# Kernel tuning notes

Hardware: AMD Instinct MI355X
Metric: run time of the kernel (lower is better)

The kernel has to match this reference:

```python
import jax, jax.numpy as jnp
import numpy as np

N_NODES = 100000
N_EDGES = 640000
H = 128

def setup_inputs() -> dict:
    key = jax.random.key(0)
    k = jax.random.split(key, 8)
    x_src = jax.random.normal(k[0], (N_NODES, H), dtype=jnp.float32)
    x_dst = jax.random.normal(k[1], (N_NODES, H), dtype=jnp.float32)
    src_idx = jax.random.randint(k[2], (N_EDGES,), 0, N_NODES, dtype=jnp.int64)
    dst_idx = jax.random.randint(k[3], (N_EDGES,), 0, N_NODES, dtype=jnp.int64)
    # torch Linear default init: U(-1/sqrt(fan_in), 1/sqrt(fan_in)); randn*scale is fine for a numeric baseline
    W1 = jax.random.normal(k[4], (H, 2 * H), dtype=jnp.float32) * (1.0 / np.sqrt(2 * H))
    b1 = jnp.zeros((H,), dtype=jnp.float32)
    W2 = jax.random.normal(k[5], (1, H), dtype=jnp.float32) * (1.0 / np.sqrt(H))
    b2 = jnp.zeros((1,), dtype=jnp.float32)
    return {"x_src": x_src, "x_dst": x_dst, "src_idx": src_idx, "dst_idx": dst_idx,
            "W1": W1, "b1": b1, "W2": W2, "b2": b2}

def reference(x_src, x_dst, src_idx, dst_idx, W1, b1, W2, b2):
    # per-edge gather of endpoint features, concat -> [E, 2H]
    h = jnp.concatenate([x_src[src_idx], x_dst[dst_idx]], axis=1)
    h = jax.nn.relu(h @ W1.T + b1)            # [E, H]
    score = (h @ W2.T + b2)[:, 0]             # [E]
    return score
```

## Files before the change

kernel.cpp:

```cpp
#include <hip/hip_runtime.h>
#include <hip/hip_bf16.h>

typedef __bf16 bf16x8 __attribute__((ext_vector_type(8)));
typedef __bf16 bf16x4 __attribute__((ext_vector_type(4)));
typedef float  f32x4  __attribute__((ext_vector_type(4)));

#define HF 128
#define W1K 256

__global__ __launch_bounds__(256, 2) void node_precompute3(
    const float* __restrict__ x_src, const float* __restrict__ x_dst,
    const float* __restrict__ W1,
    __bf16* __restrict__ u, __bf16* __restrict__ v, int nNodes)
{
    const int tid  = threadIdx.x;
    const int lane = tid & 63;
    const int wid  = tid >> 6;
    const int l15  = lane & 15;
    const int lg   = lane >> 4;

    const int gw     = blockIdx.x * 4 + wid;
    const int half   = gw & 1;
    const int stride = gridDim.x * 2;

    const float* __restrict__ x = half ? x_dst : x_src;
    const float* __restrict__ Wh = W1 + (half ? HF : 0);
    __bf16* __restrict__ outp = half ? v : u;

    bf16x8 wfrag[32];
    #pragma unroll
    for (int f = 0; f < 32; ++f) {
        const int mt = f >> 2;
        const int kk = f & 3;
        const float* p = Wh + (size_t)(mt * 16 + l15) * W1K + kk * 32 + lg * 8;
        f32x4 a = *reinterpret_cast<const f32x4*>(p);
        f32x4 b = *reinterpret_cast<const f32x4*>(p + 4);
        bf16x8 w8;
        #pragma unroll
        for (int i = 0; i < 4; ++i) {
            w8[i]     = (__bf16)a[i];
            w8[i + 4] = (__bf16)b[i];
        }
        wfrag[f] = w8;
    }

    const int nst = (nNodes + 15) >> 4;
    const size_t laneoff = (size_t)l15 * HF + lg * 8;

    int st = gw >> 1;
    if (st >= nst) return;

    f32x4 nxt[8];
    {
        const int node = min(st * 16 + l15, nNodes - 1);
        const float* rp = x + (size_t)node * HF + lg * 8;
        #pragma unroll
        for (int kk = 0; kk < 4; ++kk) {
            nxt[2 * kk]     = *reinterpret_cast<const f32x4*>(rp + kk * 32);
            nxt[2 * kk + 1] = *reinterpret_cast<const f32x4*>(rp + kk * 32 + 4);
        }
    }

    while (st < nst) {
        const int st2 = st + stride;

        bf16x8 xb[4];
        #pragma unroll
        for (int kk = 0; kk < 4; ++kk) {
            bf16x8 t;
            #pragma unroll
            for (int i = 0; i < 4; ++i) {
                t[i]     = (__bf16)nxt[2 * kk][i];
                t[i + 4] = (__bf16)nxt[2 * kk + 1][i];
            }
            xb[kk] = t;
        }

        if (st2 < nst) {
            const int node = min(st2 * 16 + l15, nNodes - 1);
            const float* rp = x + (size_t)node * HF + lg * 8;
            #pragma unroll
            for (int kk = 0; kk < 4; ++kk) {
                nxt[2 * kk]     = *reinterpret_cast<const f32x4*>(rp + kk * 32);
                nxt[2 * kk + 1] = *reinterpret_cast<const f32x4*>(rp + kk * 32 + 4);
            }
        }

        f32x4 acc[8];
        #pragma unroll
        for (int mt = 0; mt < 8; ++mt) acc[mt] = (f32x4){0.f, 0.f, 0.f, 0.f};

        #pragma unroll
        for (int kk = 0; kk < 4; ++kk)
            #pragma unroll
            for (int mt = 0; mt < 8; ++mt)
                acc[mt] = __builtin_amdgcn_mfma_f32_16x16x32_bf16(
                    wfrag[mt * 4 + kk], xb[kk], acc[mt], 0, 0, 0);

        const int mynode = st * 16 + l15;
        if (mynode < nNodes) {
            __bf16* op = outp + (size_t)mynode * HF + lg * 4;
            #pragma unroll
            for (int mt = 0; mt < 8; ++mt) {
                bf16x4 o4;
                #pragma unroll
                for (int r = 0; r < 4; ++r) o4[r] = (__bf16)acc[mt][r];
                *reinterpret_cast<bf16x4*>(op + mt * 16) = o4;
            }
        }
        st = st2;
    }
}

__global__ __launch_bounds__(256) void edge_score_kernel(
    const __bf16* __restrict__ u, const __bf16* __restrict__ v,
    const int* __restrict__ sidx, const int* __restrict__ didx,
    const float* __restrict__ W2, const float* __restrict__ b1,
    const float* __restrict__ b2,
    float* __restrict__ out, int nEdges)
{
    const int tid = threadIdx.x;
    const int sub = tid >> 4;
    const int l16 = tid & 15;

    const int ebase = blockIdx.x * 64 + sub;

    float w2v[8], b1v[8];
    #pragma unroll
    for (int j = 0; j < 8; ++j) {
        w2v[j] = W2[l16 * 8 + j];
        b1v[j] = b1[l16 * 8 + j];
    }
    const float b2v = b2[0];

    int e[4], si[4], di[4];
    #pragma unroll
    for (int q = 0; q < 4; ++q) {
        e[q] = ebase + q * 16;
        const int c = min(e[q], nEdges - 1);
        si[q] = sidx[c];
        di[q] = didx[c];
    }

    bf16x8 uv[4], vv[4];
    #pragma unroll
    for (int q = 0; q < 4; ++q) {
        uv[q] = *reinterpret_cast<const bf16x8*>(u + (size_t)si[q] * HF + l16 * 8);
        vv[q] = *reinterpret_cast<const bf16x8*>(v + (size_t)di[q] * HF + l16 * 8);
    }

    float s[4] = {0.f, 0.f, 0.f, 0.f};
    #pragma unroll
    for (int q = 0; q < 4; ++q)
        #pragma unroll
        for (int j = 0; j < 8; ++j)
            s[q] += fmaxf((float)uv[q][j] + (float)vv[q][j] + b1v[j], 0.f) * w2v[j];

    #pragma unroll
    for (int off = 1; off < 16; off <<= 1)
        #pragma unroll
        for (int q = 0; q < 4; ++q)
            s[q] += __shfl_xor(s[q], off, 64);

    if (l16 == 0) {
        #pragma unroll
        for (int q = 0; q < 4; ++q)
            if (e[q] < nEdges) out[e[q]] = s[q] + b2v;
    }
}

__global__ __launch_bounds__(256, 2) void edge_mlp_kernel(
    const float* __restrict__ x_src, const float* __restrict__ x_dst,
    const int*   __restrict__ src_idx, const int* __restrict__ dst_idx,
    const float* __restrict__ W1, const float* __restrict__ b1,
    const float* __restrict__ W2, const float* __restrict__ b2,
    float* __restrict__ out, int nEdges)
{
    __shared__ __align__(16) __bf16 w1lds[64 * 64 * 8];

    const int tid  = threadIdx.x;
    const int lane = tid & 63;
    const int wid  = tid >> 6;
    const int l15  = lane & 15;
    const int lg   = lane >> 4;

    for (int p = wid; p < 64; p += 4) {
        const int n   = p >> 3;
        const int kk  = p & 7;
        const float* src = W1 + (n * 16 + l15) * W1K + kk * 32 + lg * 8;
        bf16x8 w8;
        #pragma unroll
        for (int i = 0; i < 8; ++i) w8[i] = (__bf16)src[i];
        *reinterpret_cast<bf16x8*>(&w1lds[(p * 64 + lane) * 8]) = w8;
    }
    __syncthreads();

    float w2v[8], b1v[8];
    #pragma unroll
    for (int n = 0; n < 8; ++n) {
        w2v[n] = W2[n * 16 + l15];
        b1v[n] = b1[n * 16 + l15];
    }
    const float b2v = b2[0];

    const int ntiles = nEdges / 256;
    for (int t = blockIdx.x; t < ntiles; t += gridDim.x) {
        const int ebase = t * 256 + wid * 64;

        const float* srow[4];
        const float* drow[4];
        #pragma unroll
        for (int m = 0; m < 4; ++m) {
            const int e  = ebase + m * 16 + l15;
            srow[m] = x_src + (size_t)src_idx[e] * HF + lg * 8;
            drow[m] = x_dst + (size_t)dst_idx[e] * HF + lg * 8;
        }

        f32x4 acc[4][8];
        #pragma unroll
        for (int m = 0; m < 4; ++m)
            #pragma unroll
            for (int n = 0; n < 8; ++n)
                acc[m][n] = (f32x4){0.f, 0.f, 0.f, 0.f};

        #pragma unroll
        for (int kk = 0; kk < 8; ++kk) {
            bf16x8 a[4];
            #pragma unroll
            for (int m = 0; m < 4; ++m) {
                const float* p = (kk < 4) ? (srow[m] + kk * 32)
                                          : (drow[m] + (kk - 4) * 32);
                f32x4 u0 = *reinterpret_cast<const f32x4*>(p);
                f32x4 u1 = *reinterpret_cast<const f32x4*>(p + 4);
                bf16x8 av;
                #pragma unroll
                for (int i = 0; i < 4; ++i) {
                    av[i]     = (__bf16)u0[i];
                    av[i + 4] = (__bf16)u1[i];
                }
                a[m] = av;
            }
            #pragma unroll
            for (int n = 0; n < 8; ++n) {
                bf16x8 bfrag = *reinterpret_cast<const bf16x8*>(
                    &w1lds[((n * 8 + kk) * 64 + lane) * 8]);
                #pragma unroll
                for (int m = 0; m < 4; ++m) {
                    acc[m][n] = __builtin_amdgcn_mfma_f32_16x16x32_bf16(
                        a[m], bfrag, acc[m][n], 0, 0, 0);
                }
            }
        }

        #pragma unroll
        for (int m = 0; m < 4; ++m) {
            float part[4];
            #pragma unroll
            for (int r = 0; r < 4; ++r) {
                float s = 0.f;
                #pragma unroll
                for (int n = 0; n < 8; ++n) {
                    float hv = acc[m][n][r] + b1v[n];
                    s += fmaxf(hv, 0.f) * w2v[n];
                }
                part[r] = s;
            }
            #pragma unroll
            for (int off = 1; off < 16; off <<= 1) {
                #pragma unroll
                for (int r = 0; r < 4; ++r)
                    part[r] += __shfl_xor(part[r], off, 64);
            }
            if (l15 == m) {
                f32x4 v4 = { part[0] + b2v, part[1] + b2v,
                             part[2] + b2v, part[3] + b2v };
                *reinterpret_cast<f32x4*>(&out[ebase + m * 16 + lg * 4]) = v4;
            }
        }
    }
}

extern "C" void kernel_launch(void* const* d_in, const int* in_sizes, int n_in,
                              void* d_out, int out_size, void* d_ws, size_t ws_size,
                              hipStream_t stream) {
    const float* x_src  = (const float*)d_in[0];
    const float* x_dst  = (const float*)d_in[1];
    const int*   sidx   = (const int*)d_in[2];
    const int*   didx   = (const int*)d_in[3];
    const float* W1     = (const float*)d_in[4];
    const float* b1     = (const float*)d_in[5];
    const float* W2     = (const float*)d_in[6];
    const float* b2     = (const float*)d_in[7];
    float* out = (float*)d_out;

    const int nEdges = in_sizes[2];
    const int nNodes = in_sizes[0] / HF;

    const size_t needed = (size_t)2 * nNodes * HF * sizeof(__bf16);
    if (ws_size >= needed) {
        __bf16* u = (__bf16*)d_ws;
        __bf16* v = u + (size_t)nNodes * HF;

        node_precompute3<<<512, 256, 0, stream>>>(
            x_src, x_dst, W1, u, v, nNodes);

        const int egrid = (nEdges + 63) / 64;
        edge_score_kernel<<<egrid, 256, 0, stream>>>(
            u, v, sidx, didx, W2, b1, b2, out, nEdges);
    } else {
        edge_mlp_kernel<<<512, 256, 0, stream>>>(
            x_src, x_dst, sidx, didx, W1, b1, W2, b2, out, nEdges);
    }
}
```

Before: 86.35 us.

## Stage bf16 W1 fragments in LDS and use 512-thread node precompute blocks

Moves the bf16 weight fragments for both halves of W1 out of per-wave registers into shared memory, loaded once per block. The block grows to 8 waves, and each wave takes interleaved src/dst node tiles. Dropping 32 register fragments per lane is meant to raise occupancy and hide the latency of the streaming node-feature loads. In exchange, every MFMA now needs an LDS read of its A operand, and the fast path is limited to node counts divisible by 16, which drops the tail clamping.

```diff
diff --git a/kernel.cpp b/kernel.cpp
--- a/kernel.cpp
+++ b/kernel.cpp
@@ -8,31 +8,25 @@
 #define HF 128
 #define W1K 256
 
-__global__ __launch_bounds__(256, 2) void node_precompute3(
+__global__ __launch_bounds__(512, 4) void node_precompute4(
     const float* __restrict__ x_src, const float* __restrict__ x_dst,
     const float* __restrict__ W1,
     __bf16* __restrict__ u, __bf16* __restrict__ v, int nNodes)
 {
+    __shared__ __align__(16) __bf16 wlds[64 * 64 * 8];
+
     const int tid  = threadIdx.x;
     const int lane = tid & 63;
     const int wid  = tid >> 6;
     const int l15  = lane & 15;
     const int lg   = lane >> 4;
 
-    const int gw     = blockIdx.x * 4 + wid;
-    const int half   = gw & 1;
-    const int stride = gridDim.x * 2;
-
-    const float* __restrict__ x = half ? x_dst : x_src;
-    const float* __restrict__ Wh = W1 + (half ? HF : 0);
-    __bf16* __restrict__ outp = half ? v : u;
-
-    bf16x8 wfrag[32];
-    #pragma unroll
-    for (int f = 0; f < 32; ++f) {
-        const int mt = f >> 2;
+    for (int f = wid; f < 64; f += 8) {
+        const int h  = f >> 5;
+        const int mt = (f >> 2) & 7;
         const int kk = f & 3;
-        const float* p = Wh + (size_t)(mt * 16 + l15) * W1K + kk * 32 + lg * 8;
+        const float* p = W1 + h * HF + (size_t)(mt * 16 + l15) * W1K
+                       + kk * 32 + lg * 8;
         f32x4 a = *reinterpret_cast<const f32x4*>(p);
         f32x4 b = *reinterpret_cast<const f32x4*>(p + 4);
         bf16x8 w8;
@@ -41,19 +35,21 @@
             w8[i]     = (__bf16)a[i];
             w8[i + 4] = (__bf16)b[i];
         }
-        wfrag[f] = w8;
-    }
-
-    const int nst = (nNodes + 15) >> 4;
-    const size_t laneoff = (size_t)l15 * HF + lg * 8;
-
-    int st = gw >> 1;
-    if (st >= nst) return;
+        *reinterpret_cast<bf16x8*>(&wlds[(f * 64 + lane) * 8]) = w8;
+    }
+    __syncthreads();
+
+    const int nst    = nNodes >> 4;
+    const int T      = nst * 2;
+    const int stride = gridDim.x * 8;
+    int task = blockIdx.x * 8 + wid;
+    if (task >= T) return;
 
     f32x4 nxt[8];
     {
-        const int node = min(st * 16 + l15, nNodes - 1);
-        const float* rp = x + (size_t)node * HF + lg * 8;
+        const int h = task & 1, st = task >> 1;
+        const float* x = h ? x_dst : x_src;
+        const float* rp = x + (size_t)(st * 16 + l15) * HF + lg * 8;
         #pragma unroll
         for (int kk = 0; kk < 4; ++kk) {
             nxt[2 * kk]     = *reinterpret_cast<const f32x4*>(rp + kk * 32);
@@ -61,8 +57,9 @@
         }
     }
 
-    while (st < nst) {
-        const int st2 = st + stride;
+    while (task < T) {
+        const int h  = task & 1, st = task >> 1;
+        const int task2 = task + stride;
 
         bf16x8 xb[4];
         #pragma unroll
@@ -76,9 +73,10 @@
             xb[kk] = t;
         }
 
-        if (st2 < nst) {
-            const int node = min(st2 * 16 + l15, nNodes - 1);
-            const float* rp = x + (size_t)node * HF + lg * 8;
+        if (task2 < T) {
+            const int h2 = task2 & 1, st2 = task2 >> 1;
+            const float* x2 = h2 ? x_dst : x_src;
+            const float* rp = x2 + (size_t)(st2 * 16 + l15) * HF + lg * 8;
             #pragma unroll
             for (int kk = 0; kk < 4; ++kk) {
                 nxt[2 * kk]     = *reinterpret_cast<const f32x4*>(rp + kk * 32);
@@ -90,25 +88,26 @@
         #pragma unroll
         for (int mt = 0; mt < 8; ++mt) acc[mt] = (f32x4){0.f, 0.f, 0.f, 0.f};
 
+        const __bf16* fb = &wlds[((size_t)h * 32 * 64 + lane) * 8];
         #pragma unroll
         for (int kk = 0; kk < 4; ++kk)
             #pragma unroll
-            for (int mt = 0; mt < 8; ++mt)
+            for (int mt = 0; mt < 8; ++mt) {
+                bf16x8 wa = *reinterpret_cast<const bf16x8*>(
+                    fb + (mt * 4 + kk) * 64 * 8);
                 acc[mt] = __builtin_amdgcn_mfma_f32_16x16x32_bf16(
-                    wfrag[mt * 4 + kk], xb[kk], acc[mt], 0, 0, 0);
-
-        const int mynode = st * 16 + l15;
-        if (mynode < nNodes) {
-            __bf16* op = outp + (size_t)mynode * HF + lg * 4;
-            #pragma unroll
-            for (int mt = 0; mt < 8; ++mt) {
-                bf16x4 o4;
-                #pragma unroll
-                for (int r = 0; r < 4; ++r) o4[r] = (__bf16)acc[mt][r];
-                *reinterpret_cast<bf16x4*>(op + mt * 16) = o4;
-            }
-        }
-        st = st2;
+                    wa, xb[kk], acc[mt], 0, 0, 0);
+            }
+
+        __bf16* op = (h ? v : u) + (size_t)(st * 16 + l15) * HF + lg * 4;
+        #pragma unroll
+        for (int mt = 0; mt < 8; ++mt) {
+            bf16x4 o4;
+            #pragma unroll
+            for (int r = 0; r < 4; ++r) o4[r] = (__bf16)acc[mt][r];
+            *reinterpret_cast<bf16x4*>(op + mt * 16) = o4;
+        }
+        task = task2;
     }
 }
 
@@ -297,11 +296,11 @@
     const int nNodes = in_sizes[0] / HF;
 
     const size_t needed = (size_t)2 * nNodes * HF * sizeof(__bf16);
-    if (ws_size >= needed) {
+    if (ws_size >= needed && (nNodes & 15) == 0) {
         __bf16* u = (__bf16*)d_ws;
         __bf16* v = u + (size_t)nNodes * HF;
 
-        node_precompute3<<<512, 256, 0, stream>>>(
+        node_precompute4<<<512, 512, 0, stream>>>(
             x_src, x_dst, W1, u, v, nNodes);
 
         const int egrid = (nEdges + 63) / 64;
```

Measured after the change: 149.5 us. 73.1% more time.
